# Optimization experiments

Measured on AMD Instinct MI355X. Metric: run time of the kernel, lower is better.

Reference implementation:

```python
import jax, jax.numpy as jnp
import numpy as np

B, T, D = 2, 1024, 2048      # batch, seq_len, hidden_size
H, DK = 8, 128               # num_heads, head_k_dim
DV = 2 * DK                  # head_v_dim = head_dim * expand_v
KD, VD = H * DK, H * DV      # key_dim, value_dim
KCONV = 4                    # short conv kernel size
EPS = 1e-5


def _short_conv(x, w):
    # depthwise causal conv1d + SiLU; x: [B,T,C], w: [C,K]
    Klen = w.shape[1]
    xp = jnp.pad(x, ((0, 0), (Klen - 1, 0), (0, 0)))
    win = jnp.stack([xp[:, j:j + x.shape[1], :] for j in range(Klen)], axis=-1)  # [B,T,C,K]
    return jax.nn.silu(jnp.einsum('btck,ck->btc', win, w))


def _l2norm(x):
    return x * jax.lax.rsqrt(jnp.sum(x * x, -1, keepdims=True) + 1e-6)


def reference(hidden_states, q_w, k_w, v_w, a_w, b_w, g_w, o_w,
              q_conv_w, k_conv_w, v_conv_w, A_log, dt_bias, o_norm_w):
    h = hidden_states
    # projections + short depthwise causal conv + SiLU
    q = _short_conv(h @ q_w.T, q_conv_w)        # [B,T,KD]
    k = _short_conv(h @ k_w.T, k_conv_w)        # [B,T,KD]
    v = _short_conv(h @ v_w.T, v_conv_w)        # [B,T,VD]
    q = _l2norm(q.reshape(B, T, H, DK))
    k = _l2norm(k.reshape(B, T, H, DK))
    v = v.reshape(B, T, H, DV)
    beta = jax.nn.sigmoid(h @ b_w.T)                                 # [B,T,H]
    g = -jnp.exp(A_log) * jax.nn.softplus(h @ a_w.T + dt_bias)       # [B,T,H] decay log-gate
    scale = DK ** -0.5

    def step(S, xs):
        # S: [B,H,DK,DV] recurrent state; gated delta rule update
        qt, kt, vt, gt, bt = xs
        S = S * jnp.exp(gt)[..., None, None]
        kv = jnp.einsum('bhk,bhkv->bhv', kt, S)
        u = (vt - kv) * bt[..., None]
        S = S + jnp.einsum('bhk,bhv->bhkv', kt, u)
        ot = jnp.einsum('bhk,bhkv->bhv', qt, S) * scale
        return S, ot

    xs = (q.transpose(1, 0, 2, 3), k.transpose(1, 0, 2, 3), v.transpose(1, 0, 2, 3),
          g.transpose(1, 0, 2), beta.transpose(1, 0, 2))
    S0 = jnp.zeros((B, H, DK, DV), q.dtype)
    _, o = jax.lax.scan(step, S0, xs)
    o = o.transpose(1, 0, 2, 3)                       # [B,T,H,DV]
    # gated RMSNorm (FusedRMSNormGated) + output projection
    gate = (h @ g_w.T).reshape(B, T, H, DV)
    o = o * jax.lax.rsqrt(jnp.mean(o * o, -1, keepdims=True) + EPS) * o_norm_w
    o = o * jax.nn.silu(gate)
    return o.reshape(B, T, VD) @ o_w.T


def setup_inputs() -> dict:
    key = jax.random.key(0)
    ks = jax.random.split(key, 14)
    n = lambda i, shp, sc: jax.random.normal(ks[i], shp, jnp.float32) * sc
    return {
        'hidden_states': n(0, (B, T, D), 1.0),
        'q_w': n(1, (KD, D), 0.02), 'k_w': n(2, (KD, D), 0.02), 'v_w': n(3, (VD, D), 0.02),
        'a_w': n(4, (H, D), 0.02), 'b_w': n(5, (H, D), 0.02),
        'g_w': n(6, (VD, D), 0.02), 'o_w': n(7, (D, VD), 0.02),
        'q_conv_w': n(8, (KD, KCONV), 0.3), 'k_conv_w': n(9, (KD, KCONV), 0.3),
        'v_conv_w': n(10, (VD, KCONV), 0.3),
        'A_log': jnp.log(jax.random.uniform(ks[11], (H,), jnp.float32, 0.5, 16.0)),
        'dt_bias': n(12, (H,), 1.0),
        'o_norm_w': jnp.ones((DV,), jnp.float32),
    }
```

## Files before the change

kernel.cpp:

```cpp
#include <hip/hip_runtime.h>
#include <cstdint>

#define T_LEN 1024
#define NBIG  6400
#define SCALE_Q 0.08838834764831843f

typedef __bf16 bf16;
typedef __bf16 bf16x8 __attribute__((ext_vector_type(8)));
typedef float  f32x4  __attribute__((ext_vector_type(4)));

__device__ __forceinline__ unsigned short f2bf(float f) {
  unsigned int u = __builtin_bit_cast(unsigned int, f);
  u += 0x7FFFu + ((u >> 16) & 1u);
  return (unsigned short)(u >> 16);
}
__device__ __forceinline__ float bf2f(unsigned short u) {
  return __builtin_bit_cast(float, (unsigned int)u << 16);
}
__device__ __forceinline__ float silu_f(float x) { return x / (1.f + __expf(-x)); }

#define GLDS(src, dst) \
  __builtin_amdgcn_global_load_lds( \
      (__attribute__((address_space(1))) void*)(void*)(src), \
      (__attribute__((address_space(3))) void*)(void*)(dst), 16, 0, 0)

__global__ __launch_bounds__(256) void cvt_bf16(const float* __restrict__ in,
                                                unsigned short* __restrict__ out, int n4) {
  int idx = blockIdx.x * 256 + threadIdx.x;
  if (idx >= n4) return;
  float4 f = ((const float4*)in)[idx];
  ushort4 o = { f2bf(f.x), f2bf(f.y), f2bf(f.z), f2bf(f.w) };
  ((ushort4*)out)[idx] = o;
}

__global__ __launch_bounds__(256) void zero_f32(float* __restrict__ p, int n4) {
  int idx = blockIdx.x * 256 + threadIdx.x;
  if (idx >= n4) return;
  float4 z = {0.f, 0.f, 0.f, 0.f};
  ((float4*)p)[idx] = z;
}

__global__ __launch_bounds__(256) void build_w(
    const float* __restrict__ qw, const float* __restrict__ kw,
    const float* __restrict__ vw, const float* __restrict__ gw,
    const float* __restrict__ aw, const float* __restrict__ bw,
    unsigned short* __restrict__ W) {
  int idx = blockIdx.x * 256 + threadIdx.x;
  int r = idx >> 9;
  int c = (idx & 511) << 2;
  const float* src;
  if      (r < 1024) src = qw + (size_t)r * 2048;
  else if (r < 2048) src = kw + (size_t)(r - 1024) * 2048;
  else if (r < 4096) src = vw + (size_t)(r - 2048) * 2048;
  else if (r < 6144) src = gw + (size_t)(r - 4096) * 2048;
  else if (r < 6152) src = aw + (size_t)(r - 6144) * 2048;
  else if (r < 6160) src = bw + (size_t)(r - 6152) * 2048;
  else               src = nullptr;
  ushort4 o;
  if (src) {
    float4 f = *(const float4*)(src + c);
    o = { f2bf(f.x), f2bf(f.y), f2bf(f.z), f2bf(f.w) };
  } else {
    o = { 0, 0, 0, 0 };
  }
  *(ushort4*)(W + (size_t)r * 2048 + c) = o;
}

template <int BN, int WN, int T, bool BF16OUT, bool ATOMIC>
__global__ __launch_bounds__(T, 4) void gemm_pipe(
    const bf16* __restrict__ A, const bf16* __restrict__ Bm,
    void* __restrict__ Cv, int N, int K, int ldk) {
  constexpr int AI = (128 * 32) / (T * 8);
  constexpr int BI = (BN * 32) / (T * 8);
  constexpr int LOADS = AI + BI;
  __shared__ bf16 LA[3][128 * 32];
  __shared__ bf16 LB[3][BN * 32];
  const int tid = threadIdx.x;
  const int lane = tid & 63;
  const int wid = tid >> 6;
  const int wm = wid / WN, wn = wid % WN;
  const int bidAll = blockIdx.x;
  const int bid = ATOMIC ? (bidAll & 255) : bidAll;
  const long kofs = ATOMIC ? (long)(bidAll >> 8) * K : 0;
  const int xcd = bid & 7, jj = bid >> 3;
  const long brow = (long)(xcd + 8 * (jj & 1)) * 128;
  const long bcol = (long)(jj >> 1) * BN;

  f32x4 acc[4][4];
#pragma unroll
  for (int m = 0; m < 4; ++m)
#pragma unroll
    for (int n = 0; n < 4; ++n)
#pragma unroll
      for (int r = 0; r < 4; ++r) acc[m][n][r] = 0.f;

  const bf16* AgS[AI];
  const bf16* BgS[BI];
  int adst[AI], bdst[BI];
#pragma unroll
  for (int e = 0; e < AI; ++e) {
    const int flat = e * T + tid;
    const int row = flat >> 2;
    const int sl = (flat & 3) ^ ((row >> 1) & 3);
    AgS[e] = A + (brow + row) * (long)ldk + kofs + sl * 8;
    adst[e] = flat * 8;
  }
#pragma unroll
  for (int e = 0; e < BI; ++e) {
    const int flat = e * T + tid;
    const int row = flat >> 2;
    const int sl = (flat & 3) ^ ((row >> 1) & 3);
    BgS[e] = Bm + (bcol + row) * (long)ldk + kofs + sl * 8;
    bdst[e] = flat * 8;
  }

#define STAGE(kt, sb)                                              \
  {                                                                \
    const long ko = (long)(kt) * 32;                               \
    _Pragma("unroll")                                              \
    for (int e = 0; e < AI; ++e) GLDS(AgS[e] + ko, &LA[sb][0] + adst[e]); \
    _Pragma("unroll")                                              \
    for (int e = 0; e < BI; ++e) GLDS(BgS[e] + ko, &LB[sb][0] + bdst[e]); \
  }
#define WAIT_VM()                                                  \
  if constexpr (LOADS == 3) asm volatile("s_waitcnt vmcnt(3)" ::: "memory"); \
  else                      asm volatile("s_waitcnt vmcnt(4)" ::: "memory");

  const int r16 = lane & 15;
  const int ks = lane >> 4;
  const int pso = (ks ^ ((r16 >> 1) & 3)) * 8;
  int rdA[4], rdB[4];
#pragma unroll
  for (int i = 0; i < 4; ++i) rdA[i] = (wm * 64 + i * 16 + r16) * 32 + pso;
#pragma unroll
  for (int j = 0; j < 4; ++j) rdB[j] = (wn * 64 + j * 16 + r16) * 32 + pso;

  const int nkt = K >> 5;
  STAGE(0, 0);
  STAGE(1, 1);
  WAIT_VM();
  __builtin_amdgcn_s_barrier();

  bf16x8 af[4], bfr[4];
#pragma unroll
  for (int i = 0; i < 4; ++i) af[i] = *(const bf16x8*)(&LA[0][0] + rdA[i]);
#pragma unroll
  for (int j = 0; j < 4; ++j) bfr[j] = *(const bf16x8*)(&LB[0][0] + rdB[j]);

  for (int kt = 0; kt < nkt; ++kt) {
    const int kts = (kt + 2 < nkt) ? kt + 2 : nkt - 1;
    const int sb = (kt + 2) % 3;
    const int nb = (kt + 1) % 3;

    STAGE(kts, sb);
    __builtin_amdgcn_s_setprio(1);
#pragma unroll
    for (int i = 0; i < 4; ++i)
#pragma unroll
      for (int j = 0; j < 4; ++j)
        acc[i][j] = __builtin_amdgcn_mfma_f32_16x16x32_bf16(af[i], bfr[j], acc[i][j], 0, 0, 0);
    __builtin_amdgcn_s_setprio(0);

    asm volatile("s_waitcnt lgkmcnt(0)" ::: "memory");
    WAIT_VM();
    __builtin_amdgcn_s_barrier();
#pragma unroll
    for (int i = 0; i < 4; ++i) af[i] = *(const bf16x8*)(&LA[nb][0] + rdA[i]);
#pragma unroll
    for (int j = 0; j < 4; ++j) bfr[j] = *(const bf16x8*)(&LB[nb][0] + rdB[j]);
  }
#undef STAGE
#undef WAIT_VM

  const long row0 = brow + wm * 64 + ((lane >> 4) * 4);
  const long col0 = bcol + wn * 64 + (lane & 15);
#pragma unroll
  for (int m = 0; m < 4; ++m)
#pragma unroll
    for (int n = 0; n < 4; ++n)
#pragma unroll
      for (int r = 0; r < 4; ++r) {
        const long idx = (row0 + m * 16 + r) * (long)N + col0 + n * 16;
        if constexpr (ATOMIC)
          atomicAdd((float*)Cv + idx, acc[m][n][r]);
        else if constexpr (BF16OUT)
          ((unsigned short*)Cv)[idx] = f2bf(acc[m][n][r]);
        else
          ((float*)Cv)[idx] = acc[m][n][r];
      }
}

template <int M, int N, int K, int NW>
__device__ __forceinline__ void mm_nt_lds(const unsigned short* A, const unsigned short* B,
                                          unsigned short* outG, int ldg, int tid) {
  constexpr int NT16 = N / 16;
  constexpr int PW = (M / 16) * NT16 / NW;
  const int w = tid >> 6, l = tid & 63;
  const int row = l & 15, ko = (l >> 4) * 8;
  f32x4 acc[PW];
#pragma unroll
  for (int i = 0; i < PW; ++i)
#pragma unroll
    for (int r = 0; r < 4; ++r) acc[i][r] = 0.f;
#pragma unroll
  for (int i = 0; i < PW; ++i) {
    const int ti = w + NW * i;
    const int rt = ti / NT16, ct = ti % NT16;
#pragma unroll
    for (int kk = 0; kk < K / 32; ++kk) {
      bf16x8 af = *(const bf16x8*)(A + (rt * 16 + row) * K + kk * 32 + ko);
      bf16x8 bf = *(const bf16x8*)(B + (ct * 16 + row) * K + kk * 32 + ko);
      acc[i] = __builtin_amdgcn_mfma_f32_16x16x32_bf16(af, bf, acc[i], 0, 0, 0);
    }
  }
#pragma unroll
  for (int i = 0; i < PW; ++i) {
    const int ti = w + NW * i;
    const int rt = ti / NT16, ct = ti % NT16;
    const int r0 = rt * 16 + (l >> 4) * 4;
    const int col = ct * 16 + (l & 15);
#pragma unroll
    for (int r = 0; r < 4; ++r)
      outG[(size_t)(r0 + r) * ldg + col] = f2bf(acc[i][r]);
  }
}

template <int K>
__device__ __forceinline__ void mm64_acc(const unsigned short* A, const unsigned short* B,
                                         f32x4 acc[2], int w, int row, int ko) {
#pragma unroll
  for (int i = 0; i < 2; ++i) {
    const int ti = w + 8 * i;
    const int rt = ti >> 2, ct = ti & 3;
#pragma unroll
    for (int kk = 0; kk < K / 32; ++kk) {
      bf16x8 af = *(const bf16x8*)(A + (rt * 16 + row) * K + kk * 32 + ko);
      bf16x8 bf = *(const bf16x8*)(B + (ct * 16 + row) * K + kk * 32 + ko);
      acc[i] = __builtin_amdgcn_mfma_f32_16x16x32_bf16(af, bf, acc[i], 0, 0, 0);
    }
  }
}

__global__ __launch_bounds__(512, 1) void chunk_prep(
    const unsigned short* __restrict__ Y,
    const float* __restrict__ qcw, const float* __restrict__ kcw, const float* __restrict__ vcw,
    const float* __restrict__ A_log, const float* __restrict__ dt_bias,
    unsigned short* __restrict__ Wg, unsigned short* __restrict__ Ubg,
    unsigned short* __restrict__ Attg, unsigned short* __restrict__ Qgg,
    unsigned short* __restrict__ KgTg, float* __restrict__ decg) {
  __shared__ unsigned short Kb_s[64 * 128];
  __shared__ unsigned short Qb_s[64 * 128];
  __shared__ unsigned short VbT_s[256 * 64];
  __shared__ unsigned short Mb_s[4096];
  __shared__ unsigned short Xrow_s[2][4096];
  __shared__ unsigned short Xt_s[2][4096];
  __shared__ unsigned short Yt_s[4096];
  __shared__ float carr_s[64];
  __shared__ float beta_s[64];

  const int tid = threadIdx.x;
  const int w = tid >> 6, l = tid & 63;
  const int row16 = l & 15, ko = (l >> 4) * 8;
  const int ch = blockIdx.x;
  const int bh = ch >> 4, p = ch & 15;
  const int b = bh >> 3, h = bh & 7;
  const size_t tbase = (size_t)b * T_LEN + p * 64;
  const bool head = (p == 0);

  if (tid < 64) {
    const unsigned short* Yr = Y + (tbase + tid) * NBIG;
    float a = bf2f(Yr[6144 + h]) + dt_bias[h];
    float sp = (a > 20.f) ? a : log1pf(expf(a));
    float g = -expf(A_log[h]) * sp;
    float bp = bf2f(Yr[6152 + h]);
    beta_s[tid] = 1.f / (1.f + expf(-bp));
    float c = g;
#pragma unroll
    for (int d = 1; d < 64; d <<= 1) {
      float y = __shfl_up(c, d);
      if (tid >= d) c += y;
    }
    carr_s[tid] = c;
    if (tid == 63) decg[ch] = __expf(c);
  }
  __syncthreads();

  {
    const bool isQ = (tid < 256);
    const int wk = tid & 255;
    const int quad = wk & 31, tg = wk >> 5;
    const int c = quad * 4;
    const float* cw = isQ ? qcw : kcw;
    const int cb = (isQ ? 0 : 1024) + h * 128 + c;
    float4 wv[4];
#pragma unroll
    for (int e = 0; e < 4; ++e) wv[e] = ((const float4*)cw)[h * 128 + c + e];
    float rows[11][4];
#pragma unroll
    for (int r = 0; r < 11; ++r) {
      if (head && tg == 0 && r < 3) {
        rows[r][0] = rows[r][1] = rows[r][2] = rows[r][3] = 0.f;
      } else {
        const ushort4 x = *(const ushort4*)(Y + (tbase + tg * 8 - 3 + r) * NBIG + cb);
        rows[r][0] = bf2f(x.x); rows[r][1] = bf2f(x.y);
        rows[r][2] = bf2f(x.z); rows[r][3] = bf2f(x.w);
      }
    }
    unsigned short* dst = isQ ? Qb_s : Kb_s;
    const float sc = isQ ? SCALE_Q : 1.f;
#pragma unroll
    for (int i = 0; i < 8; ++i) {
      float acc[4], ss = 0.f;
#pragma unroll
      for (int e = 0; e < 4; ++e) {
        float a = wv[e].x * rows[i][e];
        a = fmaf(wv[e].y, rows[i + 1][e], a);
        a = fmaf(wv[e].z, rows[i + 2][e], a);
        a = fmaf(wv[e].w, rows[i + 3][e], a);
        a = silu_f(a);
        acc[e] = a;
        ss += a * a;
      }
#pragma unroll
      for (int m = 16; m >= 1; m >>= 1) ss += __shfl_xor(ss, m);
      const float rn = rsqrtf(ss + 1e-6f) * sc;
      ushort4 o = {f2bf(acc[0] * rn), f2bf(acc[1] * rn), f2bf(acc[2] * rn), f2bf(acc[3] * rn)};
      *(ushort4*)(dst + (tg * 8 + i) * 128 + c) = o;
    }
  }
  {
    const int quad = tid & 63, tg = tid >> 6;
    const int c = quad * 4;
    float4 wv[4];
#pragma unroll
    for (int e = 0; e < 4; ++e) wv[e] = ((const float4*)vcw)[h * 256 + c + e];
    float rows[11][4];
#pragma unroll
    for (int r = 0; r < 11; ++r) {
      if (head && tg == 0 && r < 3) {
        rows[r][0] = rows[r][1] = rows[r][2] = rows[r][3] = 0.f;
      } else {
        const ushort4 x = *(const ushort4*)(Y + (tbase + tg * 8 - 3 + r) * NBIG + 2048 + h * 256 + c);
        rows[r][0] = bf2f(x.x); rows[r][1] = bf2f(x.y);
        rows[r][2] = bf2f(x.z); rows[r][3] = bf2f(x.w);
      }
    }
#pragma unroll
    for (int i = 0; i < 8; ++i) {
      const int t = tg * 8 + i;
      const float bt = beta_s[t];
#pragma unroll
      for (int e = 0; e < 4; ++e) {
        float a = wv[e].x * rows[i][e];
        a = fmaf(wv[e].y, rows[i + 1][e], a);
        a = fmaf(wv[e].z, rows[i + 2][e], a);
        a = fmaf(wv[e].w, rows[i + 3][e], a);
        VbT_s[(c + e) * 64 + t] = f2bf(bt * silu_f(a));
      }
    }
  }
  __syncthreads();

  float xf[2][4];
  {
    f32x4 acc[2];
#pragma unroll
    for (int i = 0; i < 2; ++i)
#pragma unroll
      for (int r = 0; r < 4; ++r) acc[i][r] = 0.f;
    mm64_acc<128>(Kb_s, Kb_s, acc, w, row16, ko);
#pragma unroll
    for (int i = 0; i < 2; ++i) {
      const int ti = w + 8 * i;
      const int rt = ti >> 2, ct = ti & 3;
      const int r0 = rt * 16 + (l >> 4) * 4;
      const int col = ct * 16 + (l & 15);
#pragma unroll
      for (int r = 0; r < 4; ++r) {
        const int t = r0 + r, j = col;
        const float av = (j < t) ? beta_s[t] * __expf(carr_s[t] - carr_s[j]) * acc[i][r] : 0.f;
        const float dg = (t == j) ? 1.f : 0.f;
        Mb_s[t * 64 + j] = f2bf(dg + av);
        const float x0 = dg - av;
        xf[i][r] = x0;
        const unsigned short xb = f2bf(x0);
        Xrow_s[0][t * 64 + j] = xb;
        Xt_s[0][j * 64 + t] = xb;
      }
    }
  }
  __syncthreads();
  int cur = 0;
  for (int it = 0; it < 5; ++it) {
    {
      f32x4 acc[2];
#pragma unroll
      for (int i = 0; i < 2; ++i)
#pragma unroll
        for (int r = 0; r < 4; ++r) acc[i][r] = 0.f;
      mm64_acc<64>(Mb_s, Xt_s[cur], acc, w, row16, ko);
#pragma unroll
      for (int i = 0; i < 2; ++i) {
        const int ti = w + 8 * i;
        const int rt = ti >> 2, ct = ti & 3;
        const int r0 = rt * 16 + (l >> 4) * 4;
        const int col = ct * 16 + (l & 15);
#pragma unroll
        for (int r = 0; r < 4; ++r)
          Yt_s[col * 64 + (r0 + r)] = f2bf(acc[i][r]);
      }
    }
    __syncthreads();
    {
      f32x4 acc[2];
#pragma unroll
      for (int i = 0; i < 2; ++i)
#pragma unroll
        for (int r = 0; r < 4; ++r) acc[i][r] = 0.f;
      mm64_acc<64>(Xrow_s[cur], Yt_s, acc, w, row16, ko);
#pragma unroll
      for (int i = 0; i < 2; ++i) {
        const int ti = w + 8 * i;
        const int rt = ti >> 2, ct = ti & 3;
        const int r0 = rt * 16 + (l >> 4) * 4;
        const int col = ct * 16 + (l & 15);
#pragma unroll
        for (int r = 0; r < 4; ++r) {
          const float xn = 2.f * xf[i][r] - acc[i][r];
          xf[i][r] = xn;
          const unsigned short xb = f2bf(xn);
          Xrow_s[cur ^ 1][(r0 + r) * 64 + col] = xb;
          Xt_s[cur ^ 1][col * 64 + (r0 + r)] = xb;
        }
      }
    }
    cur ^= 1;
    __syncthreads();
  }
  const unsigned short* Xfin = Xrow_s[cur];
  const float ctot = carr_s[63];
  {
    f32x4 acc[2];
#pragma unroll
    for (int i = 0; i < 2; ++i)
#pragma unroll
      for (int r = 0; r < 4; ++r) acc[i][r] = 0.f;
    mm64_acc<128>(Qb_s, Kb_s, acc, w, row16, ko);
#pragma unroll
    for (int i = 0; i < 2; ++i) {
      const int ti = w + 8 * i;
      const int rt = ti >> 2, ct = ti & 3;
      const int r0 = rt * 16 + (l >> 4) * 4;
      const int col = ct * 16 + (l & 15);
#pragma unroll
      for (int r = 0; r < 4; ++r) {
        const int t = r0 + r, j = col;
        const float av = (j <= t) ? __expf(carr_s[t] - carr_s[j]) * acc[i][r] : 0.f;
        Attg[(size_t)ch * 4096 + t * 64 + j] = f2bf(av);
      }
    }
  }
#pragma unroll
  for (int i = 0; i < 16; ++i) {
    const int idx = i * 512 + tid;
    const int t = idx >> 7;
    Qgg[(size_t)ch * 8192 + idx] = f2bf(__expf(carr_s[t]) * bf2f(Qb_s[idx]));
  }
#pragma unroll
  for (int i = 0; i < 16; ++i) {
    const int idx = i * 512 + tid;
    const int d = idx >> 6, t = idx & 63;
    KgTg[(size_t)ch * 8192 + idx] = f2bf(__expf(ctot - carr_s[t]) * bf2f(Kb_s[t * 128 + d]));
  }
  __syncthreads();
  unsigned short* KbgT = Qb_s;
#pragma unroll
  for (int i = 0; i < 16; ++i) {
    const int idx = i * 512 + tid;
    const int d = idx >> 6, t = idx & 63;
    KbgT[idx] = f2bf(beta_s[t] * __expf(carr_s[t]) * bf2f(Kb_s[t * 128 + d]));
  }
  __syncthreads();
  mm_nt_lds<64, 128, 64, 8>(Xfin, KbgT, Wg + (size_t)ch * 8192, 128, tid);
  mm_nt_lds<64, 256, 64, 8>(Xfin, VbT_s, Ubg + (size_t)ch * 16384, 256, tid);
}

__device__ __forceinline__ void p2_stage(
    const unsigned short* Wg, const unsigned short* Attg, const unsigned short* Qgg,
    const unsigned short* KgTg, const unsigned short* Ubg,
    int ch, int vb, unsigned short* buf, int tid) {
#pragma unroll
  for (int i = 0; i < 2; ++i) {
    const int f = i * 512 + tid;
    GLDS(Wg + (size_t)ch * 8192 + f * 8, (char*)buf + f * 16);
  }
  {
    const int f = tid;
    GLDS(Attg + (size_t)ch * 4096 + f * 8, (char*)(buf + 8192) + f * 16);
  }
#pragma unroll
  for (int i = 0; i < 2; ++i) {
    const int f = i * 512 + tid;
    GLDS(Qgg + (size_t)ch * 8192 + f * 8, (char*)(buf + 12288) + f * 16);
  }
#pragma unroll
  for (int i = 0; i < 2; ++i) {
    const int f = i * 512 + tid;
    GLDS(KgTg + (size_t)ch * 8192 + f * 8, (char*)(buf + 20480) + f * 16);
  }
  if (tid < 128) {
    const int f = tid;
    const int t = f >> 1, c8 = f & 1;
    GLDS(Ubg + (size_t)ch * 16384 + t * 256 + vb * 16 + c8 * 8, (char*)(buf + 28672) + f * 16);
  }
}

__global__ __launch_bounds__(512, 1) void scan_chunks(
    const unsigned short* __restrict__ Wg, const unsigned short* __restrict__ Ubg,
    const unsigned short* __restrict__ Attg, const unsigned short* __restrict__ Qgg,
    const unsigned short* __restrict__ KgTg, const float* __restrict__ decg,
    float* __restrict__ osc) {
  __shared__ float StT_s[16 * 128];
  __shared__ unsigned short StTb_s[16 * 128];
  __shared__ unsigned short uT_s[16 * 64];
  __shared__ unsigned short stage_s[2][29696];

  const int tid = threadIdx.x;
  const int w = tid >> 6, l = tid & 63;
  const int row = l & 15, ko = (l >> 4) * 8;
  const int blk = blockIdx.x;
  const int vb = blk >> 4, bh = blk & 15;
  const int b = bh >> 3, h = bh & 7;
  const bool uw = (w < 4);

  for (int i = tid; i < 2048; i += 512) { StT_s[i] = 0.f; StTb_s[i] = 0; }
  p2_stage(Wg, Attg, Qgg, KgTg, Ubg, bh * 16, vb, stage_s[0], tid);

  for (int p = 0; p < 16; ++p) {
    unsigned short* bufc = stage_s[p & 1];
    const unsigned short* Wl   = bufc;
    const unsigned short* Attl = bufc + 8192;
    const unsigned short* Qgl  = bufc + 12288;
    const unsigned short* KgTl = bufc + 20480;
    const unsigned short* Ubl  = bufc + 28672;
    __syncthreads();

    f32x4 uacc;
#pragma unroll
    for (int r = 0; r < 4; ++r) uacc[r] = 0.f;
    if (uw) {
#pragma unroll
      for (int kk = 0; kk < 4; ++kk) {
        bf16x8 af = *(const bf16x8*)(Wl + (w * 16 + row) * 128 + kk * 32 + ko);
        bf16x8 bf = *(const bf16x8*)(StTb_s + row * 128 + kk * 32 + ko);
        uacc = __builtin_amdgcn_mfma_f32_16x16x32_bf16(af, bf, uacc, 0, 0, 0);
      }
      const int r0 = w * 16 + (l >> 4) * 4;
      const int col = l & 15;
#pragma unroll
      for (int r = 0; r < 4; ++r) {
        const int t = r0 + r;
        const float ubv = bf2f(Ubl[t * 16 + col]);
        uT_s[col * 64 + t] = f2bf(ubv - uacc[r]);
      }
    }
    __syncthreads();
    if (p < 15)
      p2_stage(Wg, Attg, Qgg, KgTg, Ubg, bh * 16 + p + 1, vb, stage_s[(p + 1) & 1], tid);

    f32x4 oacc;
#pragma unroll
    for (int r = 0; r < 4; ++r) oacc[r] = 0.f;
    if (uw) {
#pragma unroll
      for (int kk = 0; kk < 4; ++kk) {
        bf16x8 af = *(const bf16x8*)(Qgl + (w * 16 + row) * 128 + kk * 32 + ko);
        bf16x8 bf = *(const bf16x8*)(StTb_s + row * 128 + kk * 32 + ko);
        oacc = __builtin_amdgcn_mfma_f32_16x16x32_bf16(af, bf, oacc, 0, 0, 0);
      }
#pragma unroll
      for (int kk = 0; kk < 2; ++kk) {
        bf16x8 af = *(const bf16x8*)(Attl + (w * 16 + row) * 64 + kk * 32 + ko);
        bf16x8 bf = *(const bf16x8*)(uT_s + row * 64 + kk * 32 + ko);
        oacc = __builtin_amdgcn_mfma_f32_16x16x32_bf16(af, bf, oacc, 0, 0, 0);
      }
    }
    f32x4 sacc;
#pragma unroll
    for (int r = 0; r < 4; ++r) sacc[r] = 0.f;
#pragma unroll
    for (int kk = 0; kk < 2; ++kk) {
      bf16x8 af = *(const bf16x8*)(uT_s + row * 64 + kk * 32 + ko);
      bf16x8 bf = *(const bf16x8*)(KgTl + (w * 16 + row) * 64 + kk * 32 + ko);
      sacc = __builtin_amdgcn_mfma_f32_16x16x32_bf16(af, bf, sacc, 0, 0, 0);
    }
    const float dec = decg[bh * 16 + p];
    __syncthreads();

    if (uw) {
      const int r0 = w * 16 + (l >> 4) * 4;
      const int col = l & 15;
#pragma unroll
      for (int r = 0; r < 4; ++r) {
        const size_t trow = (size_t)b * T_LEN + p * 64 + r0 + r;
        osc[(trow * 8 + h) * 256 + vb * 16 + col] = oacc[r];
      }
    }
    {
      const int cold = w * 16 + (l & 15);
#pragma unroll
      for (int r = 0; r < 4; ++r) {
        const int idx = ((l >> 4) * 4 + r) * 128 + cold;
        const float sn = fmaf(dec, StT_s[idx], sacc[r]);
        StT_s[idx] = sn;
        StTb_s[idx] = f2bf(sn);
      }
    }
  }
}

__global__ __launch_bounds__(256) void rmsgate(
    const float* __restrict__ ob, const unsigned short* __restrict__ Y,
    const float* __restrict__ onw, unsigned short* __restrict__ Obf) {
  const int bt = blockIdx.x;
  const int tid = threadIdx.x;
  const int c = tid * 8;
  const float* orow = ob + (size_t)bt * 2048 + c;
  const unsigned short* grow = Y + (size_t)bt * NBIG + 4096 + c;
  const float4 o0 = *(const float4*)orow, o1 = *(const float4*)(orow + 4);
  const ushort4 g0 = *(const ushort4*)grow, g1 = *(const ushort4*)(grow + 4);
  const float ov[8] = {o0.x, o0.y, o0.z, o0.w, o1.x, o1.y, o1.z, o1.w};
  const float gv[8] = {bf2f(g0.x), bf2f(g0.y), bf2f(g0.z), bf2f(g0.w),
                       bf2f(g1.x), bf2f(g1.y), bf2f(g1.z), bf2f(g1.w)};
  float ss = 0.f;
#pragma unroll
  for (int e = 0; e < 8; ++e) ss += ov[e] * ov[e];
#pragma unroll
  for (int m = 16; m >= 1; m >>= 1) ss += __shfl_xor(ss, m);
  const float rn = rsqrtf(ss * (1.f / 256.f) + 1e-5f);
  const int dv = c & 255;
  unsigned short rr[8];
#pragma unroll
  for (int e = 0; e < 8; ++e) {
    const float val = ov[e] * rn * onw[dv + e] * silu_f(gv[e]);
    rr[e] = f2bf(val);
  }
  ushort4 r0 = {rr[0], rr[1], rr[2], rr[3]};
  ushort4 r1 = {rr[4], rr[5], rr[6], rr[7]};
  *(ushort4*)(Obf + (size_t)bt * 2048 + c) = r0;
  *(ushort4*)(Obf + (size_t)bt * 2048 + c + 4) = r1;
}

extern "C" void kernel_launch(void* const* d_in, const int* in_sizes, int n_in,
                              void* d_out, int out_size, void* d_ws, size_t ws_size,
                              hipStream_t stream) {
  (void)in_sizes; (void)n_in; (void)out_size; (void)ws_size;
  const float* h    = (const float*)d_in[0];
  const float* qw   = (const float*)d_in[1];
  const float* kw   = (const float*)d_in[2];
  const float* vw   = (const float*)d_in[3];
  const float* aw   = (const float*)d_in[4];
  const float* bw   = (const float*)d_in[5];
  const float* gw   = (const float*)d_in[6];
  const float* ow   = (const float*)d_in[7];
  const float* qcw  = (const float*)d_in[8];
  const float* kcw  = (const float*)d_in[9];
  const float* vcw  = (const float*)d_in[10];
  const float* Alog = (const float*)d_in[11];
  const float* dtb  = (const float*)d_in[12];
  const float* onw  = (const float*)d_in[13];

  char* ws = (char*)d_ws;
  size_t off = 0;
  auto alloc = [&](size_t bytes) {
    char* p = ws + off;
    off = (off + bytes + 255) & ~(size_t)255;
    return p;
  };
  unsigned short* hbf  = (unsigned short*)alloc(2048ull * 2048 * 2);
  unsigned short* Wb   = (unsigned short*)alloc((size_t)NBIG * 2048 * 2);
  unsigned short* owb  = (unsigned short*)alloc(2048ull * 2048 * 2);
  unsigned short* Ybf  = (unsigned short*)alloc(2048ull * NBIG * 2);
  float* osc           = (float*)alloc(2048ull * 2048 * 4);
  unsigned short* Obf  = (unsigned short*)alloc(2048ull * 2048 * 2);
  unsigned short* Wg   = (unsigned short*)alloc(256ull * 8192 * 2);
  unsigned short* Ubg  = (unsigned short*)alloc(256ull * 16384 * 2);
  unsigned short* Attg = (unsigned short*)alloc(256ull * 4096 * 2);
  unsigned short* Qgg  = (unsigned short*)alloc(256ull * 8192 * 2);
  unsigned short* KgTg = (unsigned short*)alloc(256ull * 8192 * 2);
  float* decg          = (float*)alloc(256ull * 4);

  cvt_bf16<<<4096, 256, 0, stream>>>(h, hbf, 1048576);
  build_w<<<12800, 256, 0, stream>>>(qw, kw, vw, gw, aw, bw, Wb);
  cvt_bf16<<<4096, 256, 0, stream>>>(ow, owb, 1048576);
  zero_f32<<<4096, 256, 0, stream>>>((float*)d_out, 1048576);
  gemm_pipe<256, 4, 512, true, false><<<400, 512, 0, stream>>>(
      (const bf16*)hbf, (const bf16*)Wb, Ybf, NBIG, 2048, 2048);
  chunk_prep<<<256, 512, 0, stream>>>(Ybf, qcw, kcw, vcw, Alog, dtb,
                                      Wg, Ubg, Attg, Qgg, KgTg, decg);
  scan_chunks<<<256, 512, 0, stream>>>(Wg, Ubg, Attg, Qgg, KgTg, decg, osc);
  rmsgate<<<2048, 256, 0, stream>>>(osc, Ybf, onw, Obf);
  gemm_pipe<128, 2, 256, false, true><<<512, 256, 0, stream>>>(
      (const bf16*)Obf, (const bf16*)owb, d_out, 2048, 1024, 2048);
}
```

Baseline: 220.9 us.

## Fuse prep kernels into one launch and shrink chunk_prep shared memory footprint

Merges the four preprocessing kernels (hidden bf16 conversion, weight packing, o_w conversion, output zeroing) into one launch indexed by block ranges, removing three kernel launches. In chunk_prep, the double-buffered Newton iteration buffers become single buffers guarded by an extra barrier, and the V conv/beta block moves after the iteration so VbT can alias Mb and the Xt/Yt region. This roughly halves LDS use and raises the launch-bounds occupancy hint, at the cost of one more __syncthreads per iteration. With only 256 blocks, the higher occupancy hint may matter little.

After: 215.1 us. 2.6% less time.

```diff
diff --git a/kernel.cpp b/kernel.cpp
--- a/kernel.cpp
+++ b/kernel.cpp
@@ -24,46 +24,50 @@
       (__attribute__((address_space(1))) void*)(void*)(src), \
       (__attribute__((address_space(3))) void*)(void*)(dst), 16, 0, 0)
 
-__global__ __launch_bounds__(256) void cvt_bf16(const float* __restrict__ in,
-                                                unsigned short* __restrict__ out, int n4) {
-  int idx = blockIdx.x * 256 + threadIdx.x;
-  if (idx >= n4) return;
-  float4 f = ((const float4*)in)[idx];
-  ushort4 o = { f2bf(f.x), f2bf(f.y), f2bf(f.z), f2bf(f.w) };
-  ((ushort4*)out)[idx] = o;
-}
-
-__global__ __launch_bounds__(256) void zero_f32(float* __restrict__ p, int n4) {
-  int idx = blockIdx.x * 256 + threadIdx.x;
-  if (idx >= n4) return;
-  float4 z = {0.f, 0.f, 0.f, 0.f};
-  ((float4*)p)[idx] = z;
-}
-
-__global__ __launch_bounds__(256) void build_w(
+__global__ __launch_bounds__(256) void prep_all(
+    const float* __restrict__ h, const float* __restrict__ ow,
     const float* __restrict__ qw, const float* __restrict__ kw,
     const float* __restrict__ vw, const float* __restrict__ gw,
     const float* __restrict__ aw, const float* __restrict__ bw,
-    unsigned short* __restrict__ W) {
-  int idx = blockIdx.x * 256 + threadIdx.x;
-  int r = idx >> 9;
-  int c = (idx & 511) << 2;
-  const float* src;
-  if      (r < 1024) src = qw + (size_t)r * 2048;
-  else if (r < 2048) src = kw + (size_t)(r - 1024) * 2048;
-  else if (r < 4096) src = vw + (size_t)(r - 2048) * 2048;
-  else if (r < 6144) src = gw + (size_t)(r - 4096) * 2048;
-  else if (r < 6152) src = aw + (size_t)(r - 6144) * 2048;
-  else if (r < 6160) src = bw + (size_t)(r - 6152) * 2048;
-  else               src = nullptr;
-  ushort4 o;
-  if (src) {
-    float4 f = *(const float4*)(src + c);
-    o = { f2bf(f.x), f2bf(f.y), f2bf(f.z), f2bf(f.w) };
+    unsigned short* __restrict__ hbf, unsigned short* __restrict__ owb,
+    unsigned short* __restrict__ Wb, float* __restrict__ zout) {
+  const int blk = blockIdx.x;
+  const int tid = threadIdx.x;
+  if (blk < 4096) {
+    const int idx = blk * 256 + tid;
+    float4 f = ((const float4*)h)[idx];
+    ushort4 o = { f2bf(f.x), f2bf(f.y), f2bf(f.z), f2bf(f.w) };
+    ((ushort4*)hbf)[idx] = o;
+  } else if (blk < 16896) {
+    const int idx = (blk - 4096) * 256 + tid;
+    const int r = idx >> 9;
+    const int c = (idx & 511) << 2;
+    const float* src;
+    if      (r < 1024) src = qw + (size_t)r * 2048;
+    else if (r < 2048) src = kw + (size_t)(r - 1024) * 2048;
+    else if (r < 4096) src = vw + (size_t)(r - 2048) * 2048;
+    else if (r < 6144) src = gw + (size_t)(r - 4096) * 2048;
+    else if (r < 6152) src = aw + (size_t)(r - 6144) * 2048;
+    else if (r < 6160) src = bw + (size_t)(r - 6152) * 2048;
+    else               src = nullptr;
+    ushort4 o;
+    if (src) {
+      float4 f = *(const float4*)(src + c);
+      o = { f2bf(f.x), f2bf(f.y), f2bf(f.z), f2bf(f.w) };
+    } else {
+      o = { 0, 0, 0, 0 };
+    }
+    *(ushort4*)(Wb + (size_t)r * 2048 + c) = o;
+  } else if (blk < 20992) {
+    const int idx = (blk - 16896) * 256 + tid;
+    float4 f = ((const float4*)ow)[idx];
+    ushort4 o = { f2bf(f.x), f2bf(f.y), f2bf(f.z), f2bf(f.w) };
+    ((ushort4*)owb)[idx] = o;
   } else {
-    o = { 0, 0, 0, 0 };
-  }
-  *(ushort4*)(W + (size_t)r * 2048 + c) = o;
+    const int idx = (blk - 20992) * 256 + tid;
+    float4 z = {0.f, 0.f, 0.f, 0.f};
+    ((float4*)zout)[idx] = z;
+  }
 }
 
 template <int BN, int WN, int T, bool BF16OUT, bool ATOMIC>
@@ -241,20 +245,21 @@
   }
 }
 
-__global__ __launch_bounds__(512, 1) void chunk_prep(
+__global__ __launch_bounds__(512, 4) void chunk_prep(
     const unsigned short* __restrict__ Y,
     const float* __restrict__ qcw, const float* __restrict__ kcw, const float* __restrict__ vcw,
     const float* __restrict__ A_log, const float* __restrict__ dt_bias,
     unsigned short* __restrict__ Wg, unsigned short* __restrict__ Ubg,
     unsigned short* __restrict__ Attg, unsigned short* __restrict__ Qgg,
     unsigned short* __restrict__ KgTg, float* __restrict__ decg) {
-  __shared__ unsigned short Kb_s[64 * 128];
-  __shared__ unsigned short Qb_s[64 * 128];
-  __shared__ unsigned short VbT_s[256 * 64];
-  __shared__ unsigned short Mb_s[4096];
-  __shared__ unsigned short Xrow_s[2][4096];
-  __shared__ unsigned short Xt_s[2][4096];
-  __shared__ unsigned short Yt_s[4096];
+  __shared__ unsigned short SM[36864];
+  unsigned short* Kb_s   = SM;
+  unsigned short* Qb_s   = SM + 8192;
+  unsigned short* Xrow_s = SM + 16384;
+  unsigned short* Mb_s   = SM + 20480;
+  unsigned short* Xt_s   = SM + 24576;
+  unsigned short* Yt_s   = SM + 28672;
+  unsigned short* VbT_s  = SM + 20480;
   __shared__ float carr_s[64];
   __shared__ float beta_s[64];
 
@@ -328,37 +333,6 @@
       *(ushort4*)(dst + (tg * 8 + i) * 128 + c) = o;
     }
   }
-  {
-    const int quad = tid & 63, tg = tid >> 6;
-    const int c = quad * 4;
-    float4 wv[4];
-#pragma unroll
-    for (int e = 0; e < 4; ++e) wv[e] = ((const float4*)vcw)[h * 256 + c + e];
-    float rows[11][4];
-#pragma unroll
-    for (int r = 0; r < 11; ++r) {
-      if (head && tg == 0 && r < 3) {
-        rows[r][0] = rows[r][1] = rows[r][2] = rows[r][3] = 0.f;
-      } else {
-        const ushort4 x = *(const ushort4*)(Y + (tbase + tg * 8 - 3 + r) * NBIG + 2048 + h * 256 + c);
-        rows[r][0] = bf2f(x.x); rows[r][1] = bf2f(x.y);
-        rows[r][2] = bf2f(x.z); rows[r][3] = bf2f(x.w);
-      }
-    }
-#pragma unroll
-    for (int i = 0; i < 8; ++i) {
-      const int t = tg * 8 + i;
-      const float bt = beta_s[t];
-#pragma unroll
-      for (int e = 0; e < 4; ++e) {
-        float a = wv[e].x * rows[i][e];
-        a = fmaf(wv[e].y, rows[i + 1][e], a);
-        a = fmaf(wv[e].z, rows[i + 2][e], a);
-        a = fmaf(wv[e].w, rows[i + 3][e], a);
-        VbT_s[(c + e) * 64 + t] = f2bf(bt * silu_f(a));
-      }
-    }
-  }
   __syncthreads();
 
   float xf[2][4];
@@ -384,13 +358,12 @@
         const float x0 = dg - av;
         xf[i][r] = x0;
         const unsigned short xb = f2bf(x0);
-        Xrow_s[0][t * 64 + j] = xb;
-        Xt_s[0][j * 64 + t] = xb;
+        Xrow_s[t * 64 + j] = xb;
+        Xt_s[j * 64 + t] = xb;
       }
     }
   }
   __syncthreads();
-  int cur = 0;
   for (int it = 0; it < 5; ++it) {
     {
       f32x4 acc[2];
@@ -398,7 +371,7 @@
       for (int i = 0; i < 2; ++i)
 #pragma unroll
         for (int r = 0; r < 4; ++r) acc[i][r] = 0.f;
-      mm64_acc<64>(Mb_s, Xt_s[cur], acc, w, row16, ko);
+      mm64_acc<64>(Mb_s, Xt_s, acc, w, row16, ko);
 #pragma unroll
       for (int i = 0; i < 2; ++i) {
         const int ti = w + 8 * i;
@@ -417,7 +390,8 @@
       for (int i = 0; i < 2; ++i)
 #pragma unroll
         for (int r = 0; r < 4; ++r) acc[i][r] = 0.f;
-      mm64_acc<64>(Xrow_s[cur], Yt_s, acc, w, row16, ko);
+      mm64_acc<64>(Xrow_s, Yt_s, acc, w, row16, ko);
+      __syncthreads();
 #pragma unroll
       for (int i = 0; i < 2; ++i) {
         const int ti = w + 8 * i;
@@ -429,16 +403,45 @@
           const float xn = 2.f * xf[i][r] - acc[i][r];
           xf[i][r] = xn;
           const unsigned short xb = f2bf(xn);
-          Xrow_s[cur ^ 1][(r0 + r) * 64 + col] = xb;
-          Xt_s[cur ^ 1][col * 64 + (r0 + r)] = xb;
+          Xrow_s[(r0 + r) * 64 + col] = xb;
+          Xt_s[col * 64 + (r0 + r)] = xb;
         }
       }
     }
-    cur ^= 1;
     __syncthreads();
   }
-  const unsigned short* Xfin = Xrow_s[cur];
   const float ctot = carr_s[63];
+  {
+    const int quad = tid & 63, tg = tid >> 6;
+    const int c = quad * 4;
+    float4 wv[4];
+#pragma unroll
+    for (int e = 0; e < 4; ++e) wv[e] = ((const float4*)vcw)[h * 256 + c + e];
+    float rows[11][4];
+#pragma unroll
+    for (int r = 0; r < 11; ++r) {
+      if (head && tg == 0 && r < 3) {
+        rows[r][0] = rows[r][1] = rows[r][2] = rows[r][3] = 0.f;
+      } else {
+        const ushort4 x = *(const ushort4*)(Y + (tbase + tg * 8 - 3 + r) * NBIG + 2048 + h * 256 + c);
+        rows[r][0] = bf2f(x.x); rows[r][1] = bf2f(x.y);
+        rows[r][2] = bf2f(x.z); rows[r][3] = bf2f(x.w);
+      }
+    }
+#pragma unroll
+    for (int i = 0; i < 8; ++i) {
+      const int t = tg * 8 + i;
+      const float bt = beta_s[t];
+#pragma unroll
+      for (int e = 0; e < 4; ++e) {
+        float a = wv[e].x * rows[i][e];
+        a = fmaf(wv[e].y, rows[i + 1][e], a);
+        a = fmaf(wv[e].z, rows[i + 2][e], a);
+        a = fmaf(wv[e].w, rows[i + 3][e], a);
+        VbT_s[(c + e) * 64 + t] = f2bf(bt * silu_f(a));
+      }
+    }
+  }
   {
     f32x4 acc[2];
 #pragma unroll
@@ -481,8 +484,8 @@
     KbgT[idx] = f2bf(beta_s[t] * __expf(carr_s[t]) * bf2f(Kb_s[t * 128 + d]));
   }
   __syncthreads();
-  mm_nt_lds<64, 128, 64, 8>(Xfin, KbgT, Wg + (size_t)ch * 8192, 128, tid);
-  mm_nt_lds<64, 256, 64, 8>(Xfin, VbT_s, Ubg + (size_t)ch * 16384, 256, tid);
+  mm_nt_lds<64, 128, 64, 8>(Xrow_s, KbgT, Wg + (size_t)ch * 8192, 128, tid);
+  mm_nt_lds<64, 256, 64, 8>(Xrow_s, VbT_s, Ubg + (size_t)ch * 16384, 256, tid);
 }
 
 __device__ __forceinline__ void p2_stage(
@@ -690,10 +693,8 @@
   unsigned short* KgTg = (unsigned short*)alloc(256ull * 8192 * 2);
   float* decg          = (float*)alloc(256ull * 4);
 
-  cvt_bf16<<<4096, 256, 0, stream>>>(h, hbf, 1048576);
-  build_w<<<12800, 256, 0, stream>>>(qw, kw, vw, gw, aw, bw, Wb);
-  cvt_bf16<<<4096, 256, 0, stream>>>(ow, owb, 1048576);
-  zero_f32<<<4096, 256, 0, stream>>>((float*)d_out, 1048576);
+  prep_all<<<25088, 256, 0, stream>>>(h, ow, qw, kw, vw, gw, aw, bw,
+                                      hbf, owb, Wb, (float*)d_out);
   gemm_pipe<256, 4, 512, true, false><<<400, 512, 0, stream>>>(
       (const bf16*)hbf, (const bf16*)Wb, Ybf, NBIG, 2048, 2048);
   chunk_prep<<<256, 512, 0, stream>>>(Ybf, qcw, kcw, vcw, Alog, dtb,
```
